# Kernel optimization log

Measured on AMD Instinct MI355X. Metric: run time of the kernel, lower is better.

## Reference

```python
import jax, jax.numpy as jnp
import numpy as np
from jax import lax

L = 1024       # sequence length
D = 64         # bond_dim
O = 128        # output_dim
P = 2          # d_phys
B = 4096       # batch
SPLIT = L // 2


def _ident(dl, dr):
    # identity boost added to every physical slice: t[k, p, k] += 1 for k < min(dl, dr)
    m = min(dl, dr)
    base = jnp.zeros((dl, dr), dtype=jnp.float32)
    base = base.at[jnp.arange(m), jnp.arange(m)].set(1.0)
    return base[:, None, :]  # (dl, 1, dr) broadcast over p


def setup_inputs() -> dict:
    key = jax.random.key(0)
    k0, k1, k2, k3, k4, k5 = jax.random.split(key, 6)
    x = jax.random.uniform(k0, (B, L), dtype=jnp.float32)
    left0 = jax.random.normal(k1, (1, P, D), dtype=jnp.float32) * 0.01 + _ident(1, D)
    left_rest = jax.random.normal(k2, (SPLIT - 1, D, P, D), dtype=jnp.float32) * 0.01 + _ident(D, D)[None]
    center = jax.random.normal(k3, (D, D, O), dtype=jnp.float32) / jnp.sqrt(jnp.float32(O))
    right_rest = jax.random.normal(k4, (L - SPLIT - 1, D, P, D), dtype=jnp.float32) * 0.01 + _ident(D, D)[None]
    right_last = jax.random.normal(k5, (D, P, 1), dtype=jnp.float32) * 0.01 + _ident(D, 1)
    return {"x": x, "left0": left0, "left_rest": left_rest, "center": center,
            "right_rest": right_rest, "right_last": right_last}


def _norm_env(env):
    return env / (jnp.linalg.norm(env, axis=1, keepdims=True) + 1e-8)


def reference(x, left0, left_rest, center, right_rest, right_last):
    angle = (jnp.pi / 2.0) * x
    phi = jnp.stack([jnp.cos(angle), jnp.sin(angle)], axis=-1)  # (B, L, P)

    # left sweep: first tensor has trivial left bond (=1)
    left = _norm_env(jnp.einsum('pr,bp->br', left0[0], phi[:, 0]))

    def lstep(env, inp):
        A, p = inp  # A: (D,P,D), p: (B,P)
        return _norm_env(jnp.einsum('bl,lpr,bp->br', env, A, p)), None

    phi_l = jnp.swapaxes(phi[:, 1:SPLIT], 0, 1)  # (SPLIT-1, B, P)
    left, _ = lax.scan(lstep, left, (left_rest, phi_l))

    # right sweep (from last site inward): last tensor has trivial right bond (=1)
    right = _norm_env(jnp.einsum('lp,bp->bl', right_last[:, :, 0], phi[:, L - 1]))

    def rstep(env, inp):
        A, p = inp
        return _norm_env(jnp.einsum('br,lpr,bp->bl', env, A, p)), None

    phi_r = jnp.swapaxes(phi[:, SPLIT:L - 1], 0, 1)[::-1]  # reversed order
    right, _ = lax.scan(rstep, right, (right_rest[::-1], phi_r))

    out = jnp.einsum('bl,br,lro->bo', left, right, center)  # (B, O)
    # F.normalize(p=2, dim=1) with eps=1e-12
    return out / jnp.clip(jnp.linalg.norm(out, axis=1, keepdims=True), 1e-12)
```

## Files before the change

kernel.cpp:

```cpp
#include <hip/hip_runtime.h>

typedef float vf4 __attribute__((ext_vector_type(4)));
typedef short short8 __attribute__((ext_vector_type(8)));
typedef unsigned short ushort8 __attribute__((ext_vector_type(8)));

#define LL 1024
#define DD 64
#define OO 128
#define BBATCH 4096
#define NS 511
#define SITE_F 8192

__device__ __forceinline__ void gld_lds16(const float* g, float* l) {
  __builtin_amdgcn_global_load_lds(
      (const __attribute__((address_space(1))) unsigned int*)g,
      (__attribute__((address_space(3))) unsigned int*)l, 16, 0, 0);
}

__device__ __forceinline__ void stage32k_256(float* lds, const float* g, int tid) {
#pragma unroll
  for (int q = 0; q < 8; q++) {
    const int off = (q * 256 + tid) * 4;
    gld_lds16(g + off, lds + off);
  }
}

__global__ __launch_bounds__(256) void prep(const float* __restrict__ lsrc,
                                            const float* __restrict__ rsrc,
                                            unsigned short* __restrict__ Wl,
                                            unsigned short* __restrict__ Wr) {
  __shared__ float S[SITE_F];
  const int site = blockIdx.x;
  const int dir = blockIdx.y;
  const int tid = threadIdx.x;
  const float* src = (dir ? rsrc : lsrc) + (size_t)site * SITE_F;
  unsigned short* dst = dir ? (Wr + (size_t)(NS - 1 - site) * SITE_F)
                            : (Wl + (size_t)site * SITE_F);
#pragma unroll
  for (int m = 0; m < 8; m++)
    *(vf4*)&S[(m * 256 + tid) * 4] = *(const vf4*)&src[(m * 256 + tid) * 4];
  __syncthreads();
#pragma unroll
  for (int q = 0; q < 4; q++) {
    const int slot = q * 256 + tid;
    const int lane = slot & 63, f = slot >> 6;
    const int mt = f >> 2, s = f & 3;
    const int g = lane >> 4, c = lane & 15;
    const int m = 16 * mt + c;
    ushort8 t;
#pragma unroll
    for (int j = 0; j < 8; j++) {
      const int k = 32 * s + 8 * g + j;
      float v;
      if (dir == 0) {
        const int l = k >> 1, p = k & 1;
        v = S[l * 128 + p * 64 + m] - ((m == l) ? 1.f : 0.f);
      } else {
        const int r = k >> 1, p = k & 1;
        v = S[m * 128 + p * 64 + r] - ((m == r) ? 1.f : 0.f);
      }
      const unsigned uu = __builtin_bit_cast(unsigned, v);
      t[j] = (unsigned short)((uu + 0x7FFFu + ((uu >> 16) & 1u)) >> 16);
    }
    *(ushort8*)&dst[(size_t)slot * 8] = t;
  }
}

#define BODY(I, FC, CS, SN, XV, LAST)                                          \
  {                                                                            \
    short8 e2[4];                                                              \
    _Pragma("unroll")                                                          \
    for (int s = 0; s < 4; s++) {                                              \
      int pk[4];                                                               \
      _Pragma("unroll")                                                        \
      for (int t = 0; t < 4; t++) {                                            \
        const float f0 = u[s][t] * CS, f1 = u[s][t] * SN;                      \
        int p;                                                                 \
        asm("v_cvt_pk_bf16_f32 %0, %1, %2" : "=v"(p) : "v"(f0), "v"(f1));      \
        pk[t] = p;                                                             \
      }                                                                        \
      short8 e;                                                                \
      _Pragma("unroll")                                                        \
      for (int t = 0; t < 4; t++) {                                            \
        e[2 * t] = (short)(pk[t] & 0xFFFF);                                    \
        e[2 * t + 1] = (short)((unsigned)pk[t] >> 16);                         \
      }                                                                        \
      e2[s] = e;                                                               \
    }                                                                          \
    const float keff = CS + SN;                                                \
    vf4 acc[4];                                                                \
    _Pragma("unroll")                                                          \
    for (int mt = 0; mt < 4; mt++) {                                           \
      vf4 z;                                                                   \
      z[0] = keff * u[mt][0]; z[1] = keff * u[mt][1];                          \
      z[2] = keff * u[mt][2]; z[3] = keff * u[mt][3];                          \
      acc[mt] = z;                                                             \
    }                                                                          \
    _Pragma("unroll")                                                          \
    for (int mt = 0; mt < 4; mt++) {                                           \
      acc[mt] = __builtin_amdgcn_mfma_f32_16x16x32_bf16(                       \
          __builtin_bit_cast(short8, FC[mt * 4 + 0]), e2[0], acc[mt], 0, 0, 0);\
      acc[mt] = __builtin_amdgcn_mfma_f32_16x16x32_bf16(                       \
          __builtin_bit_cast(short8, FC[mt * 4 + 1]), e2[1], acc[mt], 0, 0, 0);\
      acc[mt] = __builtin_amdgcn_mfma_f32_16x16x32_bf16(                       \
          __builtin_bit_cast(short8, FC[mt * 4 + 2]), e2[2], acc[mt], 0, 0, 0);\
      acc[mt] = __builtin_amdgcn_mfma_f32_16x16x32_bf16(                       \
          __builtin_bit_cast(short8, FC[mt * 4 + 3]), e2[3], acc[mt], 0, 0, 0);\
    }                                                                          \
    if (!(LAST)) {                                                             \
      const float xcur = XV;                                       \
      const unsigned short* Wn = W + (size_t)((I) + 2) * SITE_F;               \
      _Pragma("unroll")                                                        \
      for (int q = 0; q < 16; q++)                                             \
        FC[q] = *(const vf4*)&Wn[(q * 64 + lane) * 8];                         \
      XV = xrow[dir ? (1018 - (I)) : (5 + (I))];                   \
      __builtin_amdgcn_sched_barrier(0);                                       \
      const float qrev = 0.25f * xcur;         \
      float c_, s_;                                                            \
      asm("v_cos_f32 %0, %1" : "=v"(c_) : "v"(qrev));                          \
      asm("v_sin_f32 %0, %1" : "=v"(s_) : "v"(qrev));                          \
      CS = c_;                                                                 \
      SN = s_;                                                                 \
    }                                                                          \
    _Pragma("unroll")                                                          \
    for (int mt = 0; mt < 4; mt++) u[mt] = acc[mt];                            \
    if (((I) & 7) == 7) {         \
      float nss = 0.f;                                                         \
      _Pragma("unroll")                                                        \
      for (int mt = 0; mt < 4; mt++)                                           \
        _Pragma("unroll")                                                      \
        for (int r = 0; r < 4; r++) nss += u[mt][r] * u[mt][r];                \
      nss += __shfl_xor(nss, 16);                                              \
      nss += __shfl_xor(nss, 32);                                              \
      const int eb = (__float_as_int(nss) >> 23) & 0xFF;                       \
      const float alpha = __int_as_float((127 - ((eb - 127) >> 1)) << 23);     \
      _Pragma("unroll")                                                        \
      for (int mt = 0; mt < 4; mt++)                                           \
        _Pragma("unroll")                                                      \
        for (int r = 0; r < 4; r++) u[mt][r] *= alpha;                         \
    }                                                                          \
  }

__global__ __launch_bounds__(64, 1) void sweep(const float* __restrict__ x,
                                               const float* __restrict__ left0,
                                               const float* __restrict__ right_last,
                                               const unsigned short* __restrict__ Wl,
                                               const unsigned short* __restrict__ Wr,
                                               float* __restrict__ envL,
                                               float* __restrict__ envR) {
  const int bid = blockIdx.x;
  const int xcd = bid & 7;
  const int inner = bid >> 3;
  const int dir = xcd >> 2;
  const int pr = (xcd & 3) * 64 + inner;
  const int lane = threadIdx.x;
  const int g = lane >> 4, c = lane & 15;
  const int b = pr * 16 + c;
  const float* xrow = x + (size_t)b * LL;

  const unsigned short* W = dir ? Wr : Wl;

  vf4 u[4];
  {
    const float x0 = xrow[dir ? (LL - 1) : 0];
    const float qrev = 0.25f * x0;
    float cs, sn;
    asm("v_cos_f32 %0, %1" : "=v"(cs) : "v"(qrev));
    asm("v_sin_f32 %0, %1" : "=v"(sn) : "v"(qrev));
#pragma unroll
    for (int mt = 0; mt < 4; mt++)
#pragma unroll
      for (int r = 0; r < 4; r++) {
        const int n = 16 * mt + 4 * g + r;
        const float w0 = dir ? right_last[n * 2] : left0[n];
        const float w1 = dir ? right_last[n * 2 + 1] : left0[64 + n];
        u[mt][r] = cs * w0 + sn * w1;
      }
    float ss = 0.f;
#pragma unroll
    for (int mt = 0; mt < 4; mt++)
#pragma unroll
      for (int r = 0; r < 4; r++) ss += u[mt][r] * u[mt][r];
    ss += __shfl_xor(ss, 16);
    ss += __shfl_xor(ss, 32);
    const float a0 = 1.f / (sqrtf(ss) + 1e-8f);
#pragma unroll
    for (int mt = 0; mt < 4; mt++)
#pragma unroll
      for (int r = 0; r < 4; r++) u[mt][r] *= a0;
  }

  vf4 fA[16], fB[16];
#pragma unroll
  for (int q = 0; q < 16; q++)
    fA[q] = *(const vf4*)&W[(q * 64 + lane) * 8];
#pragma unroll
  for (int q = 0; q < 16; q++)
    fB[q] = *(const vf4*)&W[(size_t)SITE_F + (q * 64 + lane) * 8];

  float csE, snE, csO, snO;
  {
    const float q0 = 0.25f * xrow[dir ? 1022 : 1];
    asm("v_cos_f32 %0, %1" : "=v"(csE) : "v"(q0));
    asm("v_sin_f32 %0, %1" : "=v"(snE) : "v"(q0));
    const float q1 = 0.25f * xrow[dir ? 1021 : 2];
    asm("v_cos_f32 %0, %1" : "=v"(csO) : "v"(q1));
    asm("v_sin_f32 %0, %1" : "=v"(snO) : "v"(q1));
  }
  float xvA = xrow[dir ? 1020 : 3];
  float xvB = xrow[dir ? 1019 : 4];

  for (int i = 0; i < NS - 1; i += 2) {
    BODY(i, fA, csE, snE, xvA, 0)
    BODY(i + 1, fB, csO, snO, xvB, 0)
  }
  BODY(NS - 1, fA, csE, snE, xvA, 1)

  float nss = 0.f;
#pragma unroll
  for (int mt = 0; mt < 4; mt++)
#pragma unroll
    for (int r = 0; r < 4; r++) nss += u[mt][r] * u[mt][r];
  nss += __shfl_xor(nss, 16);
  nss += __shfl_xor(nss, 32);
  const float alpha = 1.f / (sqrtf(nss) + 1e-8f);

  float* eo = (dir ? envR : envL) + (size_t)b * 64;
#pragma unroll
  for (int mt = 0; mt < 4; mt++) {
    vf4 v;
#pragma unroll
    for (int r = 0; r < 4; r++) v[r] = u[mt][r] * alpha;
    *(vf4*)&eo[16 * mt + 4 * g] = v;
  }
}

__global__ __launch_bounds__(256) void centerk(const float* __restrict__ envL,
                                               const float* __restrict__ envR,
                                               const float* __restrict__ center,
                                               float* __restrict__ Pp) {
  __shared__ float Cs[2][SITE_F];
  __shared__ float LT[64 * 36];
  __shared__ float RT[64 * 36];
  const int bbase = blockIdx.x * 32;
  const int half = blockIdx.y;
  const int tid = threadIdx.x;
  const int och = tid & 31, bch = tid >> 5;
  const int o0 = och * 4, b0 = bch * 4;
#pragma unroll
  for (int m = 0; m < 8; m++) {
    const int idx = m * 256 + tid;
    const int b = idx >> 6, l = idx & 63;
    LT[l * 36 + b] = envL[(bbase + b) * 64 + l];
    RT[l * 36 + b] = envR[(bbase + b) * 64 + l];
  }
  stage32k_256(Cs[0], center + (half * 32) * SITE_F, tid);
  float acc[4][4] = {};
  for (int lh = 0; lh < 32; lh++) {
    __syncthreads();
    const int buf = lh & 1;
    if (lh + 1 < 32) stage32k_256(Cs[buf ^ 1], center + (half * 32 + lh + 1) * SITE_F, tid);
    const vf4 lv = *(const vf4*)&LT[(half * 32 + lh) * 36 + b0];
    const float* C = Cs[buf];
#pragma unroll
    for (int r = 0; r < 64; r++) {
      const vf4 rv = *(const vf4*)&RT[r * 36 + b0];
      const vf4 cv = *(const vf4*)&C[r * 128 + o0];
#pragma unroll
      for (int i2 = 0; i2 < 4; i2++) {
        const float w = lv[i2] * rv[i2];
        acc[i2][0] += w * cv[0];
        acc[i2][1] += w * cv[1];
        acc[i2][2] += w * cv[2];
        acc[i2][3] += w * cv[3];
      }
    }
  }
#pragma unroll
  for (int i2 = 0; i2 < 4; i2++) {
    vf4 v; v[0] = acc[i2][0]; v[1] = acc[i2][1]; v[2] = acc[i2][2]; v[3] = acc[i2][3];
    *(vf4*)&Pp[(size_t)half * BBATCH * 128 + (size_t)(bbase + b0 + i2) * 128 + o0] = v;
  }
}

__global__ __launch_bounds__(256) void combinek(const float* __restrict__ P,
                                                float* __restrict__ out) {
  const float* P0 = P;
  const float* P1 = P + (size_t)BBATCH * 128;
  const int row = blockIdx.x * 8 + (threadIdx.x >> 5);
  const int o0 = (threadIdx.x & 31) * 4;
  vf4 v = *(const vf4*)&P0[(size_t)row * 128 + o0];
  const vf4 v1 = *(const vf4*)&P1[(size_t)row * 128 + o0];
  v += v1;
  float ss = v[0] * v[0] + v[1] * v[1] + v[2] * v[2] + v[3] * v[3];
#pragma unroll
  for (int m = 1; m < 32; m <<= 1) ss += __shfl_xor(ss, m);
  const float inv = 1.f / fmaxf(sqrtf(ss), 1e-12f);
  v *= inv;
  *(vf4*)&out[(size_t)row * 128 + o0] = v;
}

extern "C" void kernel_launch(void* const* d_in, const int* in_sizes, int n_in,
                              void* d_out, int out_size, void* d_ws, size_t ws_size,
                              hipStream_t stream) {
  const float* x = (const float*)d_in[0];
  const float* left0 = (const float*)d_in[1];
  const float* left_rest = (const float*)d_in[2];
  const float* center = (const float*)d_in[3];
  const float* right_rest = (const float*)d_in[4];
  const float* right_last = (const float*)d_in[5];
  float* out = (float*)d_out;

  char* wsb = (char*)d_ws;
  unsigned short* Wl = (unsigned short*)wsb;
  unsigned short* Wr = Wl + (size_t)NS * SITE_F;
  float* envL = (float*)(Wr + (size_t)NS * SITE_F);
  float* envR = envL + (size_t)BBATCH * 64;
  float* Pp = envR + (size_t)BBATCH * 64;

  hipLaunchKernelGGL(prep, dim3(NS, 2), dim3(256), 0, stream,
                     left_rest, right_rest, Wl, Wr);
  hipLaunchKernelGGL(sweep, dim3(512), dim3(64), 0, stream,
                     x, left0, right_last, Wl, Wr, envL, envR);
  hipLaunchKernelGGL(centerk, dim3(BBATCH / 32, 2), dim3(256), 0, stream,
                     envL, envR, center, Pp);
  hipLaunchKernelGGL(combinek, dim3(BBATCH / 8), dim3(256), 0, stream, Pp, out);
}
```

Measured before the change: 381.8 us.

## Stream site weights and inputs through an LDS ring with async global-to-LDS loads

Replaces the two register-resident weight fragment buffers with a 4-slot LDS ring filled by global_load_lds three sites ahead, using explicit vmcnt waits. Input x values are staged into LDS in 64-site chunks instead of being loaded per step from global memory. The idea is to deepen the prefetch and free VGPRs. In exchange, every step adds LDS reads to the serial dependency chain. The diff also packs the bf16 operands with a bit_cast instead of per-element shuffles.

```diff
diff --git a/kernel.cpp b/kernel.cpp
--- a/kernel.cpp
+++ b/kernel.cpp
@@ -1,6 +1,7 @@
 #include <hip/hip_runtime.h>
 
 typedef float vf4 __attribute__((ext_vector_type(4)));
+typedef int vi4 __attribute__((ext_vector_type(4)));
 typedef short short8 __attribute__((ext_vector_type(8)));
 typedef unsigned short ushort8 __attribute__((ext_vector_type(8)));
 
@@ -15,6 +16,11 @@
   __builtin_amdgcn_global_load_lds(
       (const __attribute__((address_space(1))) unsigned int*)g,
       (__attribute__((address_space(3))) unsigned int*)l, 16, 0, 0);
+}
+__device__ __forceinline__ void gld_lds4(const float* g, float* l) {
+  __builtin_amdgcn_global_load_lds(
+      (const __attribute__((address_space(1))) unsigned int*)g,
+      (__attribute__((address_space(3))) unsigned int*)l, 4, 0, 0);
 }
 
 __device__ __forceinline__ void stage32k_256(float* lds, const float* g, int tid) {
@@ -66,8 +72,36 @@
   }
 }
 
-#define BODY(I, FC, CS, SN, XV, LAST)                                          \
+#define STAGE(SLOT, SITE)                                                      \
   {                                                                            \
+    const float* Ws_ = Wf + (size_t)(SITE) * 4096;                             \
+    float* d_ = &ring[SLOT][0];                                                \
+    _Pragma("unroll")                                                          \
+    for (int q = 0; q < 16; q++)                                               \
+      gld_lds16(Ws_ + q * 256 + lane * 4, d_ + q * 256 + lane * 4);            \
+  }
+
+#define STAGE_X(C)                                                             \
+  {                                                                            \
+    float* xd_ = &xls[(C) & 1][0];                                             \
+    _Pragma("unroll")                                                          \
+    for (int q = 0; q < 16; q++) {                                             \
+      const int tl_ = q * 4 + g;                                               \
+      const int st_ = 64 * (C) + tl_;                                          \
+      const int ti_ = dir ? (1022 - st_) : (1 + st_);                          \
+      gld_lds4(xrow + ti_, xd_ + q * 64 + lane);                               \
+    }                                                                          \
+  }
+
+#define BODY(I, VCS)                                                           \
+  {                                                                            \
+    asm volatile("s_waitcnt vmcnt(" VCS ")" ::: "memory");                     \
+    __builtin_amdgcn_sched_barrier(0);                                         \
+    const float* rb = &ring[(I) & 3][0];                                       \
+    vf4 FC[16];                                                                \
+    _Pragma("unroll")                                                          \
+    for (int q = 0; q < 16; q++)                                               \
+      FC[q] = *(const vf4*)&rb[q * 256 + lane * 4];                            \
     short8 e2[4];                                                              \
     _Pragma("unroll")                                                          \
     for (int s = 0; s < 4; s++) {                                              \
@@ -79,13 +113,7 @@
         asm("v_cvt_pk_bf16_f32 %0, %1, %2" : "=v"(p) : "v"(f0), "v"(f1));      \
         pk[t] = p;                                                             \
       }                                                                        \
-      short8 e;                                                                \
-      _Pragma("unroll")                                                        \
-      for (int t = 0; t < 4; t++) {                                            \
-        e[2 * t] = (short)(pk[t] & 0xFFFF);                                    \
-        e[2 * t + 1] = (short)((unsigned)pk[t] >> 16);                         \
-      }                                                                        \
-      e2[s] = e;                                                               \
+      e2[s] = __builtin_bit_cast(short8, (vi4){pk[0], pk[1], pk[2], pk[3]});   \
     }                                                                          \
     const float keff = CS + SN;                                                \
     vf4 acc[4];                                                                \
@@ -107,15 +135,13 @@
       acc[mt] = __builtin_amdgcn_mfma_f32_16x16x32_bf16(                       \
           __builtin_bit_cast(short8, FC[mt * 4 + 3]), e2[3], acc[mt], 0, 0, 0);\
     }                                                                          \
-    if (!(LAST)) {                                                             \
-      const float xcur = XV;                                       \
-      const unsigned short* Wn = W + (size_t)((I) + 2) * SITE_F;               \
-      _Pragma("unroll")                                                        \
-      for (int q = 0; q < 16; q++)                                             \
-        FC[q] = *(const vf4*)&Wn[(q * 64 + lane) * 8];                         \
-      XV = xrow[dir ? (1018 - (I)) : (5 + (I))];                   \
-      __builtin_amdgcn_sched_barrier(0);                                       \
-      const float qrev = 0.25f * xcur;         \
+    if ((I) + 3 <= NS - 1) { STAGE(((I) + 3) & 3, (I) + 3) }                   \
+    if (((I) & 63) == 48 && (I) <= 432) { STAGE_X(((I) >> 6) + 1) }            \
+    __builtin_amdgcn_sched_barrier(0);                                         \
+    if ((I) <= NS - 2) {         \
+      const int nI = (I) + 1;                                                  \
+      const float xv = xls[(nI >> 6) & 1][(nI & 63) * 16 + c];                 \
+      const float qrev = 0.25f * xv;                                           \
       float c_, s_;                                                            \
       asm("v_cos_f32 %0, %1" : "=v"(c_) : "v"(qrev));                          \
       asm("v_sin_f32 %0, %1" : "=v"(s_) : "v"(qrev));                          \
@@ -148,17 +174,18 @@
                                                const unsigned short* __restrict__ Wr,
                                                float* __restrict__ envL,
                                                float* __restrict__ envR) {
+  __shared__ float ring[4][4096];
+  __shared__ float xls[2][1024];
   const int bid = blockIdx.x;
   const int xcd = bid & 7;
-  const int inner = bid >> 3;
   const int dir = xcd >> 2;
-  const int pr = (xcd & 3) * 64 + inner;
+  const int pr = (xcd & 3) * 64 + (bid >> 3);
   const int lane = threadIdx.x;
   const int g = lane >> 4, c = lane & 15;
   const int b = pr * 16 + c;
   const float* xrow = x + (size_t)b * LL;
 
-  const unsigned short* W = dir ? Wr : Wl;
+  const float* Wf = (const float*)(dir ? Wr : Wl);
 
   vf4 u[4];
   {
@@ -190,31 +217,27 @@
       for (int r = 0; r < 4; r++) u[mt][r] *= a0;
   }
 
-  vf4 fA[16], fB[16];
-#pragma unroll
-  for (int q = 0; q < 16; q++)
-    fA[q] = *(const vf4*)&W[(q * 64 + lane) * 8];
-#pragma unroll
-  for (int q = 0; q < 16; q++)
-    fB[q] = *(const vf4*)&W[(size_t)SITE_F + (q * 64 + lane) * 8];
-
-  float csE, snE, csO, snO;
+  STAGE_X(0)
+  STAGE(0, 0)
+  STAGE(1, 1)
+  STAGE(2, 2)
+  asm volatile("s_waitcnt vmcnt(48)" ::: "memory");
+  __builtin_amdgcn_sched_barrier(0);
+
+  float CS, SN;
   {
-    const float q0 = 0.25f * xrow[dir ? 1022 : 1];
-    asm("v_cos_f32 %0, %1" : "=v"(csE) : "v"(q0));
-    asm("v_sin_f32 %0, %1" : "=v"(snE) : "v"(q0));
-    const float q1 = 0.25f * xrow[dir ? 1021 : 2];
-    asm("v_cos_f32 %0, %1" : "=v"(csO) : "v"(q1));
-    asm("v_sin_f32 %0, %1" : "=v"(snO) : "v"(q1));
-  }
-  float xvA = xrow[dir ? 1020 : 3];
-  float xvB = xrow[dir ? 1019 : 4];
-
-  for (int i = 0; i < NS - 1; i += 2) {
-    BODY(i, fA, csE, snE, xvA, 0)
-    BODY(i + 1, fB, csO, snO, xvB, 0)
-  }
-  BODY(NS - 1, fA, csE, snE, xvA, 1)
+    const float xv = xls[0][c];
+    const float qrev = 0.25f * xv;
+    asm("v_cos_f32 %0, %1" : "=v"(CS) : "v"(qrev));
+    asm("v_sin_f32 %0, %1" : "=v"(SN) : "v"(qrev));
+  }
+
+  for (int i = 0; i < NS - 3; i++) {
+    BODY(i, "32")
+  }
+  BODY(NS - 3, "32")
+  BODY(NS - 2, "16")
+  BODY(NS - 1, "0")
 
   float nss = 0.f;
 #pragma unroll
```

After: 508.3 us. 33.1% more time.

## Stage site weights through LDS ring shared by two waves per block

Applied to the files above, without the earlier changes.

The sweep kernel now uses 128-thread blocks with two waves, each handling its own 16-sample batch. Groups of four site weight tiles are staged into a double-buffered LDS ring with global_load_lds and read from LDS per step, so two waves share one global fetch instead of each wave holding two sites in registers. The cost is a __syncthreads every four sites, LDS read latency on the critical MFMA chain, and half as many blocks (256 instead of 512), which could leave CUs underused. The bf16 packing of the environment is also simplified to a single bit cast.

```diff
diff --git a/kernel.cpp b/kernel.cpp
--- a/kernel.cpp
+++ b/kernel.cpp
@@ -1,6 +1,7 @@
 #include <hip/hip_runtime.h>
 
 typedef float vf4 __attribute__((ext_vector_type(4)));
+typedef int vi4 __attribute__((ext_vector_type(4)));
 typedef short short8 __attribute__((ext_vector_type(8)));
 typedef unsigned short ushort8 __attribute__((ext_vector_type(8)));
 
@@ -66,8 +67,30 @@
   }
 }
 
-#define BODY(I, FC, CS, SN, XV, LAST)                                          \
+#define STAGE_GROUP(G, BUF)                                                    \
   {                                                                            \
+    _Pragma("unroll")                                                          \
+    for (int s4 = 0; s4 < 4; s4++) {                                           \
+      int st_ = (G) * 4 + s4;                                                  \
+      if (st_ > NS - 1) st_ = NS - 1;                                          \
+      const float* Ws_ = Wf + (size_t)st_ * 4096;                              \
+      float* d_ = &ring[BUF][s4][0];                                           \
+      _Pragma("unroll")                                                        \
+      for (int q = 0; q < 8; q++)                                              \
+        gld_lds16(Ws_ + q * 512 + tid * 4, d_ + q * 512 + tid * 4);            \
+    }                                                                          \
+  }
+
+#define BODY(I, BUF, S4)                                                       \
+  {                                                                            \
+    const float* rb = &ring[BUF][S4][0];                                       \
+    vf4 FC[16];                                                                \
+    _Pragma("unroll")                                                          \
+    for (int q = 0; q < 16; q++)                                               \
+      FC[q] = *(const vf4*)&rb[(q * 64 + lane) * 4];                           \
+    const int nI = (I) + 1;                                                    \
+    float xn = 0.f;                                                            \
+    if (nI <= NS - 1) xn = xrow[dir ? (1022 - nI) : (1 + nI)];                 \
     short8 e2[4];                                                              \
     _Pragma("unroll")                                                          \
     for (int s = 0; s < 4; s++) {                                              \
@@ -79,13 +102,7 @@
         asm("v_cvt_pk_bf16_f32 %0, %1, %2" : "=v"(p) : "v"(f0), "v"(f1));      \
         pk[t] = p;                                                             \
       }                                                                        \
-      short8 e;                                                                \
-      _Pragma("unroll")                                                        \
-      for (int t = 0; t < 4; t++) {                                            \
-        e[2 * t] = (short)(pk[t] & 0xFFFF);                                    \
-        e[2 * t + 1] = (short)((unsigned)pk[t] >> 16);                         \
-      }                                                                        \
-      e2[s] = e;                                                               \
+      e2[s] = __builtin_bit_cast(short8, (vi4){pk[0], pk[1], pk[2], pk[3]});   \
     }                                                                          \
     const float keff = CS + SN;                                                \
     vf4 acc[4];                                                                \
@@ -107,23 +124,16 @@
       acc[mt] = __builtin_amdgcn_mfma_f32_16x16x32_bf16(                       \
           __builtin_bit_cast(short8, FC[mt * 4 + 3]), e2[3], acc[mt], 0, 0, 0);\
     }                                                                          \
-    if (!(LAST)) {                                                             \
-      const float xcur = XV;                                       \
-      const unsigned short* Wn = W + (size_t)((I) + 2) * SITE_F;               \
-      _Pragma("unroll")                                                        \
-      for (int q = 0; q < 16; q++)                                             \
-        FC[q] = *(const vf4*)&Wn[(q * 64 + lane) * 8];                         \
-      XV = xrow[dir ? (1018 - (I)) : (5 + (I))];                   \
-      __builtin_amdgcn_sched_barrier(0);                                       \
-      const float qrev = 0.25f * xcur;         \
+    _Pragma("unroll")                                                          \
+    for (int mt = 0; mt < 4; mt++) u[mt] = acc[mt];                            \
+    if (nI <= NS - 1) {                                   \
+      const float qrev = 0.25f * xn;           \
       float c_, s_;                                                            \
       asm("v_cos_f32 %0, %1" : "=v"(c_) : "v"(qrev));                          \
       asm("v_sin_f32 %0, %1" : "=v"(s_) : "v"(qrev));                          \
       CS = c_;                                                                 \
       SN = s_;                                                                 \
     }                                                                          \
-    _Pragma("unroll")                                                          \
-    for (int mt = 0; mt < 4; mt++) u[mt] = acc[mt];                            \
     if (((I) & 7) == 7) {         \
       float nss = 0.f;                                                         \
       _Pragma("unroll")                                                        \
@@ -141,24 +151,26 @@
     }                                                                          \
   }
 
-__global__ __launch_bounds__(64, 1) void sweep(const float* __restrict__ x,
-                                               const float* __restrict__ left0,
-                                               const float* __restrict__ right_last,
-                                               const unsigned short* __restrict__ Wl,
-                                               const unsigned short* __restrict__ Wr,
-                                               float* __restrict__ envL,
-                                               float* __restrict__ envR) {
+__global__ __launch_bounds__(128, 1) void sweep(const float* __restrict__ x,
+                                                const float* __restrict__ left0,
+                                                const float* __restrict__ right_last,
+                                                const unsigned short* __restrict__ Wl,
+                                                const unsigned short* __restrict__ Wr,
+                                                float* __restrict__ envL,
+                                                float* __restrict__ envR) {
+  __shared__ float ring[2][4][4096];
   const int bid = blockIdx.x;
   const int xcd = bid & 7;
-  const int inner = bid >> 3;
   const int dir = xcd >> 2;
-  const int pr = (xcd & 3) * 64 + inner;
-  const int lane = threadIdx.x;
-  const int g = lane >> 4, c = lane & 15;
-  const int b = pr * 16 + c;
+  const int slot = (xcd & 3) * 32 + (bid >> 3);
+  const int tid = threadIdx.x;
+  const int wave = tid >> 6;
+  const int lane = tid & 63;
+  const int g_ = lane >> 4, c = lane & 15;
+  const int b = (slot * 2 + wave) * 16 + c;
   const float* xrow = x + (size_t)b * LL;
 
-  const unsigned short* W = dir ? Wr : Wl;
+  const float* Wf = (const float*)(dir ? Wr : Wl);
 
   vf4 u[4];
   {
@@ -171,7 +183,7 @@
     for (int mt = 0; mt < 4; mt++)
 #pragma unroll
       for (int r = 0; r < 4; r++) {
-        const int n = 16 * mt + 4 * g + r;
+        const int n = 16 * mt + 4 * g_ + r;
         const float w0 = dir ? right_last[n * 2] : left0[n];
         const float w1 = dir ? right_last[n * 2 + 1] : left0[64 + n];
         u[mt][r] = cs * w0 + sn * w1;
@@ -190,31 +202,29 @@
       for (int r = 0; r < 4; r++) u[mt][r] *= a0;
   }
 
-  vf4 fA[16], fB[16];
-#pragma unroll
-  for (int q = 0; q < 16; q++)
-    fA[q] = *(const vf4*)&W[(q * 64 + lane) * 8];
-#pragma unroll
-  for (int q = 0; q < 16; q++)
-    fB[q] = *(const vf4*)&W[(size_t)SITE_F + (q * 64 + lane) * 8];
-
-  float csE, snE, csO, snO;
+  float CS, SN;
   {
     const float q0 = 0.25f * xrow[dir ? 1022 : 1];
-    asm("v_cos_f32 %0, %1" : "=v"(csE) : "v"(q0));
-    asm("v_sin_f32 %0, %1" : "=v"(snE) : "v"(q0));
-    const float q1 = 0.25f * xrow[dir ? 1021 : 2];
-    asm("v_cos_f32 %0, %1" : "=v"(csO) : "v"(q1));
-    asm("v_sin_f32 %0, %1" : "=v"(snO) : "v"(q1));
-  }
-  float xvA = xrow[dir ? 1020 : 3];
-  float xvB = xrow[dir ? 1019 : 4];
-
-  for (int i = 0; i < NS - 1; i += 2) {
-    BODY(i, fA, csE, snE, xvA, 0)
-    BODY(i + 1, fB, csO, snO, xvB, 0)
-  }
-  BODY(NS - 1, fA, csE, snE, xvA, 1)
+    asm("v_cos_f32 %0, %1" : "=v"(CS) : "v"(q0));
+    asm("v_sin_f32 %0, %1" : "=v"(SN) : "v"(q0));
+  }
+
+  STAGE_GROUP(0, 0)
+  __syncthreads();
+
+  for (int g = 0; g < 127; g++) {
+    const int buf = g & 1;
+    STAGE_GROUP(g + 1, buf ^ 1)
+    const int i0 = g * 4;
+    BODY(i0 + 0, buf, 0)
+    BODY(i0 + 1, buf, 1)
+    BODY(i0 + 2, buf, 2)
+    BODY(i0 + 3, buf, 3)
+    __syncthreads();
+  }
+  BODY(508, 1, 0)
+  BODY(509, 1, 1)
+  BODY(510, 1, 2)
 
   float nss = 0.f;
 #pragma unroll
@@ -231,7 +241,7 @@
     vf4 v;
 #pragma unroll
     for (int r = 0; r < 4; r++) v[r] = u[mt][r] * alpha;
-    *(vf4*)&eo[16 * mt + 4 * g] = v;
+    *(vf4*)&eo[16 * mt + 4 * g_] = v;
   }
 }
 
@@ -320,7 +330,7 @@
 
   hipLaunchKernelGGL(prep, dim3(NS, 2), dim3(256), 0, stream,
                      left_rest, right_rest, Wl, Wr);
-  hipLaunchKernelGGL(sweep, dim3(512), dim3(64), 0, stream,
+  hipLaunchKernelGGL(sweep, dim3(256), dim3(128), 0, stream,
                      x, left0, right_last, Wl, Wr, envL, envR);
   hipLaunchKernelGGL(centerk, dim3(BBATCH / 32, 2), dim3(256), 0, stream,
                      envL, envR, center, Pp);
```

Measured after the change: 387.6 us. Within noise of the previous version (+1.5%).
